# Kernel optimization log

Hardware: AMD Instinct MI355X
Metric: run time of the kernel (lower is better)

## Reference

```python
import jax, jax.numpy as jnp
import numpy as np

N = 100000   # nodes
E = 1600000  # edges
DIN, H, C = 64, 64, 40


def setup_inputs() -> dict:
    key = jax.random.key(0)
    ks = jax.random.split(key, 8)
    x = jax.random.normal(ks[0], (N, DIN), dtype=jnp.float32)
    edge_index = jax.random.randint(ks[1], (2, E), 0, N, dtype=jnp.int64)
    def glorot(k, fan_in, fan_out):
        s = jnp.sqrt(6.0 / (fan_in + fan_out)).astype(jnp.float32)
        return jax.random.uniform(k, (fan_in, fan_out), jnp.float32, -s, s)
    return {
        "x": x,
        "edge_index": edge_index,
        "W1": glorot(ks[2], DIN, H), "b1": jnp.zeros((H,), jnp.float32),
        "W2": glorot(ks[3], H, H),   "b2": jnp.zeros((H,), jnp.float32),
        "W3": glorot(ks[4], H, C),   "b3": jnp.zeros((C,), jnp.float32),
    }


def _gcn_norm(edge_index, n_nodes):
    # PyG GCNConv default: add self-loops, symmetric normalization.
    loop = jnp.arange(n_nodes, dtype=edge_index.dtype)
    src = jnp.concatenate([edge_index[0], loop])  # [E+N]
    dst = jnp.concatenate([edge_index[1], loop])
    deg = jax.ops.segment_sum(jnp.ones_like(dst, dtype=jnp.float32), dst,
                              num_segments=n_nodes)
    dinv = jnp.where(deg > 0, jax.lax.rsqrt(deg), 0.0)
    norm = dinv[src] * dinv[dst]  # [E+N]
    return src, dst, norm


def _gcn_conv(x, src, dst, norm, W, b, n_nodes):
    h = x @ W                                   # [N, F_out] tiny GEMM
    msg = h[src] * norm[:, None]                # gather + scale  [E+N, F_out]
    out = jax.ops.segment_sum(msg, dst, num_segments=n_nodes)  # scatter-add
    return out + b


def reference(x, edge_index, W1, b1, W2, b2, W3, b3):
    n = x.shape[0]
    src, dst, norm = _gcn_norm(edge_index, n)
    h = jax.nn.relu(_gcn_conv(x, src, dst, norm, W1, b1, n))
    # dropout(p=0.5) is identity in eval mode
    h = jax.nn.relu(_gcn_conv(h, src, dst, norm, W2, b2, n))
    return _gcn_conv(h, src, dst, norm, W3, b3, n)
```

## Files before the change

### kernel.cpp

```cpp
#include <hip/hip_runtime.h>
#include <hip/hip_fp16.h>

#define NN 100000
#define NE 1600000
#define NPAD 100352
#define ST 68
#define SXS 68
#define NB 256
#define CE (NE / NB)
#define D1 391
#define L1 (D1 * NB)


__global__ __launch_bounds__(256) void k_hist(const int* __restrict__ dst,
                                              unsigned* __restrict__ H) {
    __shared__ unsigned h[D1];
    int b = blockIdx.x, t = threadIdx.x;
    for (int i = t; i < D1; i += 256) h[i] = 0;
    __syncthreads();
    int beg = b * CE, end = beg + CE;
    for (int i = beg + t; i < end; i += 256)
        atomicAdd(&h[((unsigned)dst[i]) >> 8], 1u);
    __syncthreads();
    for (int d = t; d < D1; d += 256) H[d * NB + b] = h[d];
}

__global__ __launch_bounds__(256) void k_scanA(const unsigned* __restrict__ in,
                                               unsigned* __restrict__ bsum, int L) {
    __shared__ unsigned sp[256];
    int i = blockIdx.x * 256 + threadIdx.x;
    sp[threadIdx.x] = (i < L) ? in[i] : 0;
    __syncthreads();
    for (int off = 128; off > 0; off >>= 1) {
        if (threadIdx.x < off) sp[threadIdx.x] += sp[threadIdx.x + off];
        __syncthreads();
    }
    if (threadIdx.x == 0) bsum[blockIdx.x] = sp[0];
}

__global__ __launch_bounds__(512) void k_scanB(unsigned* __restrict__ bsum, int nb) {
    __shared__ unsigned sp[512];
    int t = threadIdx.x;
    unsigned v = (t < nb) ? bsum[t] : 0;
    sp[t] = v;
    __syncthreads();
    for (int off = 1; off < 512; off <<= 1) {
        unsigned u = (t >= off) ? sp[t - off] : 0;
        __syncthreads();
        sp[t] += u;
        __syncthreads();
    }
    if (t < nb) bsum[t] = sp[t] - v;
}

__global__ __launch_bounds__(256) void k_scanC(unsigned* __restrict__ H,
                                               const unsigned* __restrict__ bsum, int L) {
    __shared__ unsigned sp[256];
    int t = threadIdx.x, i = blockIdx.x * 256 + t;
    unsigned v = (i < L) ? H[i] : 0;
    sp[t] = v;
    __syncthreads();
    for (int off = 1; off < 256; off <<= 1) {
        unsigned u = (t >= off) ? sp[t - off] : 0;
        __syncthreads();
        sp[t] += u;
        __syncthreads();
    }
    if (i < L) H[i] = bsum[blockIdx.x] + sp[t] - v;
}

__global__ __launch_bounds__(256) void k_scat(const int* __restrict__ src,
                                              const int* __restrict__ dst,
                                              const unsigned* __restrict__ H,
                                              unsigned* __restrict__ pairs) {
    __shared__ unsigned base[D1];
    __shared__ unsigned run[D1];
    int b = blockIdx.x, t = threadIdx.x;
    for (int d = t; d < D1; d += 256) { base[d] = H[d * NB + b]; run[d] = 0; }
    __syncthreads();
    int beg = b * CE, end = beg + CE;
    for (int i = beg + t; i < end; i += 256) {
        unsigned dv = (unsigned)dst[i];
        unsigned d = dv >> 8;
        unsigned r = atomicAdd(&run[d], 1u);
        pairs[base[d] + r] = ((dv & 255u) << 24) | (unsigned)src[i];
    }
}

__global__ __launch_bounds__(256) void k_bucket(const unsigned* __restrict__ H,
                                                const unsigned* __restrict__ pairs,
                                                int* __restrict__ rowptr,
                                                float* __restrict__ dinv,
                                                int* __restrict__ csr) {
    __shared__ unsigned h[256], sc[256], run[256];
    int b = blockIdx.x, t = threadIdx.x;
    unsigned S = H[b * NB];
    unsigned Send = (b + 1 < D1) ? H[(b + 1) * NB] : NE;
    h[t] = 0; run[t] = 0;
    __syncthreads();
    for (unsigned i = S + t; i < Send; i += 256)
        atomicAdd(&h[pairs[i] >> 24], 1u);
    __syncthreads();
    unsigned v = h[t];
    sc[t] = v;
    __syncthreads();
    for (int off = 1; off < 256; off <<= 1) {
        unsigned u = (t >= off) ? sc[t - off] : 0;
        __syncthreads();
        sc[t] += u;
        __syncthreads();
    }
    unsigned ex = sc[t] - v;
    int node = (b << 8) + t;
    if (node < NN) {
        rowptr[node] = (int)(S + ex);
        dinv[node] = rsqrtf((float)v + 1.0f);
    }
    if (b == 0 && t == 0) rowptr[NN] = NE;
    sc[t] = ex;
    __syncthreads();
    for (unsigned i = S + t; i < Send; i += 256) {
        unsigned p = pairs[i];
        unsigned k = p >> 24;
        unsigned r = atomicAdd(&run[k], 1u);
        csr[S + sc[k] + r] = (int)(p & 0xFFFFFFu);
    }
}


__global__ __launch_bounds__(256, 4) void k_gemm1(const float* __restrict__ A,
                                                  const float* __restrict__ W,
                                                  const float* __restrict__ dinv,
                                                  __half* __restrict__ out, int n) {
    __shared__ float sX[32 * SXS];
    __shared__ float sW[64 * 64];
    int row0 = blockIdx.x * 32;
    for (int i = threadIdx.x; i < 16 * 64; i += 256)
        ((float4*)sW)[i] = ((const float4*)W)[i];
    for (int i = threadIdx.x; i < 32 * 16; i += 256) {
        int r = i >> 4, c4 = i & 15;
        int row = row0 + r;
        float4 v = (row < n) ? ((const float4*)(A + ((size_t)row << 6)))[c4]
                             : make_float4(0.f, 0.f, 0.f, 0.f);
        *(float4*)&sX[r * SXS + (c4 << 2)] = v;
    }
    __syncthreads();

    int ci = (threadIdx.x & 15) * 4;
    int r0 = (threadIdx.x >> 4) * 2;
    float acc[2][4] = {};
#pragma unroll 16
    for (int k = 0; k < 64; ++k) {
        float a0 = sX[r0 * SXS + k];
        float a1 = sX[(r0 + 1) * SXS + k];
        float4 w = *(const float4*)&sW[(k << 6) + ci];
        acc[0][0] += a0 * w.x; acc[0][1] += a0 * w.y;
        acc[0][2] += a0 * w.z; acc[0][3] += a0 * w.w;
        acc[1][0] += a1 * w.x; acc[1][1] += a1 * w.y;
        acc[1][2] += a1 * w.z; acc[1][3] += a1 * w.w;
    }
#pragma unroll
    for (int rr = 0; rr < 2; ++rr) {
        int row = row0 + r0 + rr;
        if (row < n) {
            float di = dinv[row];
            union { uint2 u; __half2 h[2]; } P;
            P.h[0] = __float22half2_rn(make_float2(acc[rr][0] * di, acc[rr][1] * di));
            P.h[1] = __float22half2_rn(make_float2(acc[rr][2] * di, acc[rr][3] * di));
            *(uint2*)(out + ((size_t)row << 6) + ci) = P.u;
        }
    }
}


#define ACC8(r) { \
    const __half2* hh_ = (const __half2*)&(r); \
    float2 f_; \
    f_ = __half22float2(hh_[0]); a[0].x += f_.x; a[0].y += f_.y; \
    f_ = __half22float2(hh_[1]); a[1].x += f_.x; a[1].y += f_.y; \
    f_ = __half22float2(hh_[2]); a[2].x += f_.x; a[2].y += f_.y; \
    f_ = __half22float2(hh_[3]); a[3].x += f_.x; a[3].y += f_.y; }

template <int MODE>
__global__ __launch_bounds__(256) void k_agg(const int* __restrict__ rowptr,
                                             const int* __restrict__ csr,
                                             const __half* __restrict__ g,
                                             const float* __restrict__ dinv,
                                             const float* __restrict__ bias,
                                             const float* __restrict__ Wn,
                                             const float* __restrict__ bias2,
                                             void* __restrict__ outv, int n) {
    constexpr int M = (MODE == 3) ? 40 : 64;
    __shared__ float sW[(MODE >= 2) ? 64 * M : 1];
    __shared__ float sT[(MODE >= 2) ? 32 * ST : 1];
    int tid = threadIdx.x;
    if (MODE >= 2) {
        for (int i = tid; i < 16 * M; i += 256)
            ((float4*)sW)[i] = ((const float4*)Wn)[i];
    }
    int n0 = blockIdx.x << 5;
    int lane = tid & 63, wid = tid >> 6;
    int ng = lane >> 3, fl = lane & 7;
    int nl = (wid << 3) + ng;
    int node = n0 + nl;
    bool valid = node < n;
    const uint4* g4 = (const uint4*)g;

    int beg = 0, end = 0;
    if (valid) { beg = rowptr[node]; end = rowptr[node + 1]; }
    float2 a[4] = {};
    int j = beg;
    for (; j + 4 <= end; j += 4) {
        int s0 = csr[j], s1 = csr[j + 1], s2 = csr[j + 2], s3 = csr[j + 3];
        uint4 r0 = g4[((size_t)s0 << 3) + fl];
        uint4 r1 = g4[((size_t)s1 << 3) + fl];
        uint4 r2 = g4[((size_t)s2 << 3) + fl];
        uint4 r3 = g4[((size_t)s3 << 3) + fl];
        ACC8(r0); ACC8(r1); ACC8(r2); ACC8(r3);
    }
    for (; j < end; ++j) {
        int s = csr[j];
        uint4 r = g4[((size_t)s << 3) + fl];
        ACC8(r);
    }
    if (valid) {
        uint4 r = g4[((size_t)node << 3) + fl];
        ACC8(r);
    }
    float di = valid ? dinv[node] : 0.f;
    float t[8] = { a[0].x, a[0].y, a[1].x, a[1].y, a[2].x, a[2].y, a[3].x, a[3].y };

    if (MODE == 1) {
        if (valid) {
            float4 b0 = *(const float4*)(bias + (fl << 3));
            float4 b1 = *(const float4*)(bias + (fl << 3) + 4);
            float bv[8] = { b0.x, b0.y, b0.z, b0.w, b1.x, b1.y, b1.z, b1.w };
            union { uint4 u; __half2 h[4]; } P;
#pragma unroll
            for (int k = 0; k < 4; ++k) {
                float o0 = fmaxf(t[2 * k]     * di + bv[2 * k],     0.f) * di;
                float o1 = fmaxf(t[2 * k + 1] * di + bv[2 * k + 1], 0.f) * di;
                P.h[k] = __float22half2_rn(make_float2(o0, o1));
            }
            ((uint4*)outv)[((size_t)node << 3) + fl] = P.u;
        }
        return;
    }

    {
        float4 b0 = make_float4(0.f, 0.f, 0.f, 0.f), b1 = b0;
        if (MODE == 2) {
            b0 = *(const float4*)(bias + (fl << 3));
            b1 = *(const float4*)(bias + (fl << 3) + 4);
        }
        float bv[8] = { b0.x, b0.y, b0.z, b0.w, b1.x, b1.y, b1.z, b1.w };
        float* row = &sT[nl * ST + (fl << 3)];
#pragma unroll
        for (int k = 0; k < 8; ++k) {
            float v = t[k] * di;
            if (MODE == 2) v = fmaxf(v + bv[k], 0.f);
            row[k] = v;
        }
    }
    __syncthreads();

    int rg = tid >> 4;
    int cq = (tid & 15) << 2;
    if (cq < M) {
        float s0[4] = {}, s1[4] = {};
#pragma unroll 8
        for (int k = 0; k < 64; ++k) {
            float4 w = *(const float4*)&sW[k * M + cq];
            float a0 = sT[(rg * 2) * ST + k];
            float a1 = sT[(rg * 2 + 1) * ST + k];
            s0[0] += a0 * w.x; s0[1] += a0 * w.y; s0[2] += a0 * w.z; s0[3] += a0 * w.w;
            s1[0] += a1 * w.x; s1[1] += a1 * w.y; s1[2] += a1 * w.z; s1[3] += a1 * w.w;
        }
#pragma unroll
        for (int r = 0; r < 2; ++r) {
            float* s = (r == 0) ? s0 : s1;
            int node2 = n0 + rg * 2 + r;
            if (node2 < n) {
                if (MODE == 2) {
                    float d2 = dinv[node2];
                    union { uint2 u; __half2 h[2]; } P;
                    P.h[0] = __float22half2_rn(make_float2(s[0] * d2, s[1] * d2));
                    P.h[1] = __float22half2_rn(make_float2(s[2] * d2, s[3] * d2));
                    *(uint2*)((__half*)outv + ((size_t)node2 << 6) + cq) = P.u;
                } else {
                    float4 o = make_float4(s[0] + bias2[cq],     s[1] + bias2[cq + 1],
                                           s[2] + bias2[cq + 2], s[3] + bias2[cq + 3]);
                    *(float4*)((float*)outv + (size_t)node2 * 40 + cq) = o;
                }
            }
        }
    }
}

extern "C" void kernel_launch(void* const* d_in, const int* in_sizes, int n_in,
                              void* d_out, int out_size, void* d_ws, size_t ws_size,
                              hipStream_t stream) {
    const float* x  = (const float*)d_in[0];
    const int*   ei = (const int*)d_in[1];
    const float* W1 = (const float*)d_in[2];
    const float* b1 = (const float*)d_in[3];
    const float* W2 = (const float*)d_in[4];
    const float* b2 = (const float*)d_in[5];
    const float* W3 = (const float*)d_in[6];
    const float* b3 = (const float*)d_in[7];
    float* out = (float*)d_out;

    const int* src = ei;
    const int* dst = ei + NE;

    unsigned* H      = (unsigned*)d_ws;
    unsigned* bsum   = H + L1;
    int*      rowptr = (int*)(bsum + 512);
    float*    dinv   = (float*)(rowptr + NPAD);
    unsigned* pairs  = (unsigned*)(dinv + NPAD);
    int*      csr    = (int*)(pairs + NE);
    __half*   gA     = (__half*)(csr + NE);
    __half*   gB     = gA + (size_t)NN * 64;

    const int B = 256;
    const int gG = (NN + 31) / 32;
    const int gAgg = (NN + 31) / 32;
    const int nScan = (L1 + 255) / 256;

    k_hist<<<NB, B, 0, stream>>>(dst, H);
    k_scanA<<<nScan, B, 0, stream>>>(H, bsum, L1);
    k_scanB<<<1, 512, 0, stream>>>(bsum, nScan);
    k_scanC<<<nScan, B, 0, stream>>>(H, bsum, L1);
    k_scat<<<NB, B, 0, stream>>>(src, dst, H, pairs);
    k_bucket<<<D1, B, 0, stream>>>(H, pairs, rowptr, dinv, csr);

    k_gemm1<<<gG, B, 0, stream>>>(x, W1, dinv, gA, NN);
    k_agg<2><<<gAgg, B, 0, stream>>>(rowptr, csr, gA, dinv, b1, W2, nullptr, gB, NN);
    k_agg<1><<<gAgg, B, 0, stream>>>(rowptr, csr, gB, dinv, b2, nullptr, nullptr, gA, NN);
    k_agg<3><<<gAgg, B, 0, stream>>>(rowptr, csr, gA, dinv, nullptr, W3, b3, out, NN);
}
```

Baseline: 184.5 us.

## Degree-sort nodes within buckets to balance aggregation work and unroll gathers by eight

k_bucket now bitonic-sorts the 256 nodes of each bucket by in-degree and emits a permutation plus per-position begin/end edge ranges. The three aggregation kernels walk nodes in that order, so nodes of similar degree share a wavefront and lanes diverge less, and the output rows are scattered through the permutation. The gather loop is also unrolled to 8 edges to keep more loads in flight. The costs are a sort inside the bucket kernel, an extra indirection, and scattered writes that no longer land on contiguous rows.

```diff
diff --git a/kernel.cpp b/kernel.cpp
--- a/kernel.cpp
+++ b/kernel.cpp
@@ -91,8 +91,10 @@
                                                 const unsigned* __restrict__ pairs,
                                                 int* __restrict__ rowptr,
                                                 float* __restrict__ dinv,
-                                                int* __restrict__ csr) {
-    __shared__ unsigned h[256], sc[256], run[256];
+                                                int* __restrict__ csr,
+                                                int* __restrict__ order,
+                                                int2* __restrict__ begend) {
+    __shared__ unsigned h[256], sc[256], run[256], key[256];
     int b = blockIdx.x, t = threadIdx.x;
     unsigned S = H[b * NB];
     unsigned Send = (b + 1 < D1) ? H[(b + 1) * NB] : NE;
@@ -118,6 +120,7 @@
     }
     if (b == 0 && t == 0) rowptr[NN] = NE;
     sc[t] = ex;
+    key[t] = (node < NN) ? ((v << 8) | (unsigned)t) : 0xFFFFFFFFu;
     __syncthreads();
     for (unsigned i = S + t; i < Send; i += 256) {
         unsigned p = pairs[i];
@@ -125,6 +128,25 @@
         unsigned r = atomicAdd(&run[k], 1u);
         csr[S + sc[k] + r] = (int)(p & 0xFFFFFFu);
     }
+    for (int kk = 2; kk <= 256; kk <<= 1) {
+        for (int jj = kk >> 1; jj > 0; jj >>= 1) {
+            __syncthreads();
+            int p = t ^ jj;
+            if (p > t) {
+                unsigned a = key[t], c = key[p];
+                bool up = ((t & kk) == 0);
+                if ((a > c) == up) { key[t] = c; key[p] = a; }
+            }
+        }
+    }
+    __syncthreads();
+    unsigned kv = key[t];
+    int nl2 = (int)(kv & 255u);
+    int dg = (int)(kv >> 8);
+    int pos = (b << 8) + t;
+    order[pos] = (b << 8) + nl2;
+    int bg = (int)(S + sc[nl2]);
+    begend[pos] = make_int2(bg, bg + dg);
 }
 
 
@@ -182,7 +204,8 @@
     f_ = __half22float2(hh_[3]); a[3].x += f_.x; a[3].y += f_.y; }
 
 template <int MODE>
-__global__ __launch_bounds__(256) void k_agg(const int* __restrict__ rowptr,
+__global__ __launch_bounds__(256) void k_agg(const int* __restrict__ order,
+                                             const int2* __restrict__ begend,
                                              const int* __restrict__ csr,
                                              const __half* __restrict__ g,
                                              const float* __restrict__ dinv,
@@ -202,21 +225,40 @@
     int lane = tid & 63, wid = tid >> 6;
     int ng = lane >> 3, fl = lane & 7;
     int nl = (wid << 3) + ng;
-    int node = n0 + nl;
-    bool valid = node < n;
+    int pos = n0 + nl;
+    bool valid = pos < n;
+    int node = 0, beg = 0, end = 0;
+    if (valid) {
+        node = order[pos];
+        int2 be = begend[pos];
+        beg = be.x; end = be.y;
+    }
     const uint4* g4 = (const uint4*)g;
 
-    int beg = 0, end = 0;
-    if (valid) { beg = rowptr[node]; end = rowptr[node + 1]; }
     float2 a[4] = {};
     int j = beg;
-    for (; j + 4 <= end; j += 4) {
+    for (; j + 8 <= end; j += 8) {
+        int s0 = csr[j],     s1 = csr[j + 1], s2 = csr[j + 2], s3 = csr[j + 3];
+        int s4 = csr[j + 4], s5 = csr[j + 5], s6 = csr[j + 6], s7 = csr[j + 7];
+        uint4 r0 = g4[((size_t)s0 << 3) + fl];
+        uint4 r1 = g4[((size_t)s1 << 3) + fl];
+        uint4 r2 = g4[((size_t)s2 << 3) + fl];
+        uint4 r3 = g4[((size_t)s3 << 3) + fl];
+        uint4 r4 = g4[((size_t)s4 << 3) + fl];
+        uint4 r5 = g4[((size_t)s5 << 3) + fl];
+        uint4 r6 = g4[((size_t)s6 << 3) + fl];
+        uint4 r7 = g4[((size_t)s7 << 3) + fl];
+        ACC8(r0); ACC8(r1); ACC8(r2); ACC8(r3);
+        ACC8(r4); ACC8(r5); ACC8(r6); ACC8(r7);
+    }
+    if (j + 4 <= end) {
         int s0 = csr[j], s1 = csr[j + 1], s2 = csr[j + 2], s3 = csr[j + 3];
         uint4 r0 = g4[((size_t)s0 << 3) + fl];
         uint4 r1 = g4[((size_t)s1 << 3) + fl];
         uint4 r2 = g4[((size_t)s2 << 3) + fl];
         uint4 r3 = g4[((size_t)s3 << 3) + fl];
         ACC8(r0); ACC8(r1); ACC8(r2); ACC8(r3);
+        j += 4;
     }
     for (; j < end; ++j) {
         int s = csr[j];
@@ -279,8 +321,9 @@
 #pragma unroll
         for (int r = 0; r < 2; ++r) {
             float* s = (r == 0) ? s0 : s1;
-            int node2 = n0 + rg * 2 + r;
-            if (node2 < n) {
+            int pos2 = n0 + rg * 2 + r;
+            if (pos2 < n) {
+                int node2 = order[pos2];
                 if (MODE == 2) {
                     float d2 = dinv[node2];
                     union { uint2 u; __half2 h[2]; } P;
@@ -317,7 +360,9 @@
     unsigned* bsum   = H + L1;
     int*      rowptr = (int*)(bsum + 512);
     float*    dinv   = (float*)(rowptr + NPAD);
-    unsigned* pairs  = (unsigned*)(dinv + NPAD);
+    int*      order  = (int*)(dinv + NPAD);
+    int2*     begend = (int2*)(order + NPAD);
+    unsigned* pairs  = (unsigned*)(begend + NPAD);
     int*      csr    = (int*)(pairs + NE);
     __half*   gA     = (__half*)(csr + NE);
     __half*   gB     = gA + (size_t)NN * 64;
@@ -332,10 +377,10 @@
     k_scanB<<<1, 512, 0, stream>>>(bsum, nScan);
     k_scanC<<<nScan, B, 0, stream>>>(H, bsum, L1);
     k_scat<<<NB, B, 0, stream>>>(src, dst, H, pairs);
-    k_bucket<<<D1, B, 0, stream>>>(H, pairs, rowptr, dinv, csr);
+    k_bucket<<<D1, B, 0, stream>>>(H, pairs, rowptr, dinv, csr, order, begend);
 
     k_gemm1<<<gG, B, 0, stream>>>(x, W1, dinv, gA, NN);
-    k_agg<2><<<gAgg, B, 0, stream>>>(rowptr, csr, gA, dinv, b1, W2, nullptr, gB, NN);
-    k_agg<1><<<gAgg, B, 0, stream>>>(rowptr, csr, gB, dinv, b2, nullptr, nullptr, gA, NN);
-    k_agg<3><<<gAgg, B, 0, stream>>>(rowptr, csr, gA, dinv, nullptr, W3, b3, out, NN);
-}
+    k_agg<2><<<gAgg, B, 0, stream>>>(order, begend, csr, gA, dinv, b1, W2, nullptr, gB, NN);
+    k_agg<1><<<gAgg, B, 0, stream>>>(order, begend, csr, gB, dinv, b2, nullptr, nullptr, gA, NN);
+    k_agg<3><<<gAgg, B, 0, stream>>>(order, begend, csr, gA, dinv, nullptr, W3, b3, out, NN);
+}
```

New measurement: 206.7 us. 12.1% more time.

## Apply W3 before final aggregation to gather 40-wide rows instead of 64

Applied to the files above, without the earlier changes.

Reorders the last layer so the W3 projection is fused into the second aggregation kernel, producing a 40-wide half-precision intermediate. A new aggregation kernel then gathers the narrower 40-feature rows and adds the bias, cutting the gather traffic of the last layer. The cost is that 3 of 8 lanes per node sit idle in the final gather, and rows are 80 bytes, which are not 128-byte aligned. It also needs an extra workspace buffer.

```diff
diff --git a/kernel.cpp b/kernel.cpp
--- a/kernel.cpp
+++ b/kernel.cpp
@@ -181,23 +181,19 @@
     f_ = __half22float2(hh_[2]); a[2].x += f_.x; a[2].y += f_.y; \
     f_ = __half22float2(hh_[3]); a[3].x += f_.x; a[3].y += f_.y; }
 
-template <int MODE>
-__global__ __launch_bounds__(256) void k_agg(const int* __restrict__ rowptr,
-                                             const int* __restrict__ csr,
-                                             const __half* __restrict__ g,
-                                             const float* __restrict__ dinv,
-                                             const float* __restrict__ bias,
-                                             const float* __restrict__ Wn,
-                                             const float* __restrict__ bias2,
-                                             void* __restrict__ outv, int n) {
-    constexpr int M = (MODE == 3) ? 40 : 64;
-    __shared__ float sW[(MODE >= 2) ? 64 * M : 1];
-    __shared__ float sT[(MODE >= 2) ? 32 * ST : 1];
+template <int M>
+__global__ __launch_bounds__(256) void k_agg64(const int* __restrict__ rowptr,
+                                               const int* __restrict__ csr,
+                                               const __half* __restrict__ g,
+                                               const float* __restrict__ dinv,
+                                               const float* __restrict__ bias,
+                                               const float* __restrict__ Wn,
+                                               __half* __restrict__ outh, int n) {
+    __shared__ float sW[64 * M];
+    __shared__ float sT[32 * ST];
     int tid = threadIdx.x;
-    if (MODE >= 2) {
-        for (int i = tid; i < 16 * M; i += 256)
-            ((float4*)sW)[i] = ((const float4*)Wn)[i];
-    }
+    for (int i = tid; i < 16 * M; i += 256)
+        ((float4*)sW)[i] = ((const float4*)Wn)[i];
     int n0 = blockIdx.x << 5;
     int lane = tid & 63, wid = tid >> 6;
     int ng = lane >> 3, fl = lane & 7;
@@ -230,37 +226,14 @@
     float di = valid ? dinv[node] : 0.f;
     float t[8] = { a[0].x, a[0].y, a[1].x, a[1].y, a[2].x, a[2].y, a[3].x, a[3].y };
 
-    if (MODE == 1) {
-        if (valid) {
-            float4 b0 = *(const float4*)(bias + (fl << 3));
-            float4 b1 = *(const float4*)(bias + (fl << 3) + 4);
-            float bv[8] = { b0.x, b0.y, b0.z, b0.w, b1.x, b1.y, b1.z, b1.w };
-            union { uint4 u; __half2 h[4]; } P;
-#pragma unroll
-            for (int k = 0; k < 4; ++k) {
-                float o0 = fmaxf(t[2 * k]     * di + bv[2 * k],     0.f) * di;
-                float o1 = fmaxf(t[2 * k + 1] * di + bv[2 * k + 1], 0.f) * di;
-                P.h[k] = __float22half2_rn(make_float2(o0, o1));
-            }
-            ((uint4*)outv)[((size_t)node << 3) + fl] = P.u;
-        }
-        return;
-    }
-
     {
-        float4 b0 = make_float4(0.f, 0.f, 0.f, 0.f), b1 = b0;
-        if (MODE == 2) {
-            b0 = *(const float4*)(bias + (fl << 3));
-            b1 = *(const float4*)(bias + (fl << 3) + 4);
-        }
+        float4 b0 = *(const float4*)(bias + (fl << 3));
+        float4 b1 = *(const float4*)(bias + (fl << 3) + 4);
         float bv[8] = { b0.x, b0.y, b0.z, b0.w, b1.x, b1.y, b1.z, b1.w };
         float* row = &sT[nl * ST + (fl << 3)];
 #pragma unroll
-        for (int k = 0; k < 8; ++k) {
-            float v = t[k] * di;
-            if (MODE == 2) v = fmaxf(v + bv[k], 0.f);
-            row[k] = v;
-        }
+        for (int k = 0; k < 8; ++k)
+            row[k] = fmaxf(t[k] * di + bv[k], 0.f);
     }
     __syncthreads();
 
@@ -281,19 +254,62 @@
             float* s = (r == 0) ? s0 : s1;
             int node2 = n0 + rg * 2 + r;
             if (node2 < n) {
-                if (MODE == 2) {
-                    float d2 = dinv[node2];
-                    union { uint2 u; __half2 h[2]; } P;
-                    P.h[0] = __float22half2_rn(make_float2(s[0] * d2, s[1] * d2));
-                    P.h[1] = __float22half2_rn(make_float2(s[2] * d2, s[3] * d2));
-                    *(uint2*)((__half*)outv + ((size_t)node2 << 6) + cq) = P.u;
-                } else {
-                    float4 o = make_float4(s[0] + bias2[cq],     s[1] + bias2[cq + 1],
-                                           s[2] + bias2[cq + 2], s[3] + bias2[cq + 3]);
-                    *(float4*)((float*)outv + (size_t)node2 * 40 + cq) = o;
-                }
+                float d2 = dinv[node2];
+                union { uint2 u; __half2 h[2]; } P;
+                P.h[0] = __float22half2_rn(make_float2(s[0] * d2, s[1] * d2));
+                P.h[1] = __float22half2_rn(make_float2(s[2] * d2, s[3] * d2));
+                *(uint2*)(outh + (size_t)node2 * M + cq) = P.u;
             }
         }
+    }
+}
+
+
+__global__ __launch_bounds__(256) void k_agg40(const int* __restrict__ rowptr,
+                                               const int* __restrict__ csr,
+                                               const __half* __restrict__ q,
+                                               const float* __restrict__ dinv,
+                                               const float* __restrict__ bias,
+                                               float* __restrict__ out, int n) {
+    int tid = threadIdx.x;
+    int n0 = blockIdx.x << 5;
+    int lane = tid & 63, wid = tid >> 6;
+    int ng = lane >> 3, fl = lane & 7;
+    int nl = (wid << 3) + ng;
+    int node = n0 + nl;
+    bool valid = (node < n) && (fl < 5);
+
+    int beg = 0, end = 0;
+    if (valid) { beg = rowptr[node]; end = rowptr[node + 1]; }
+    float2 a[4] = {};
+    int j = beg;
+    for (; j + 4 <= end; j += 4) {
+        int s0 = csr[j], s1 = csr[j + 1], s2 = csr[j + 2], s3 = csr[j + 3];
+        uint4 r0 = *(const uint4*)(q + (size_t)s0 * 40 + (fl << 3));
+        uint4 r1 = *(const uint4*)(q + (size_t)s1 * 40 + (fl << 3));
+        uint4 r2 = *(const uint4*)(q + (size_t)s2 * 40 + (fl << 3));
+        uint4 r3 = *(const uint4*)(q + (size_t)s3 * 40 + (fl << 3));
+        ACC8(r0); ACC8(r1); ACC8(r2); ACC8(r3);
+    }
+    for (; j < end; ++j) {
+        int s = csr[j];
+        uint4 r = *(const uint4*)(q + (size_t)s * 40 + (fl << 3));
+        ACC8(r);
+    }
+    if (valid) {
+        uint4 r = *(const uint4*)(q + (size_t)node * 40 + (fl << 3));
+        ACC8(r);
+        float di = dinv[node];
+        float t[8] = { a[0].x, a[0].y, a[1].x, a[1].y, a[2].x, a[2].y, a[3].x, a[3].y };
+        float4 b0 = *(const float4*)(bias + (fl << 3));
+        float4 b1 = *(const float4*)(bias + (fl << 3) + 4);
+        float4 o0 = make_float4(t[0] * di + b0.x, t[1] * di + b0.y,
+                                t[2] * di + b0.z, t[3] * di + b0.w);
+        float4 o1 = make_float4(t[4] * di + b1.x, t[5] * di + b1.y,
+                                t[6] * di + b1.z, t[7] * di + b1.w);
+        float* op = out + (size_t)node * 40 + (fl << 3);
+        *(float4*)op = o0;
+        *(float4*)(op + 4) = o1;
     }
 }
 
@@ -321,6 +337,7 @@
     int*      csr    = (int*)(pairs + NE);
     __half*   gA     = (__half*)(csr + NE);
     __half*   gB     = gA + (size_t)NN * 64;
+    __half*   gC     = gB + (size_t)NN * 64;
 
     const int B = 256;
     const int gG = (NN + 31) / 32;
@@ -335,7 +352,7 @@
     k_bucket<<<D1, B, 0, stream>>>(H, pairs, rowptr, dinv, csr);
 
     k_gemm1<<<gG, B, 0, stream>>>(x, W1, dinv, gA, NN);
-    k_agg<2><<<gAgg, B, 0, stream>>>(rowptr, csr, gA, dinv, b1, W2, nullptr, gB, NN);
-    k_agg<1><<<gAgg, B, 0, stream>>>(rowptr, csr, gB, dinv, b2, nullptr, nullptr, gA, NN);
-    k_agg<3><<<gAgg, B, 0, stream>>>(rowptr, csr, gA, dinv, nullptr, W3, b3, out, NN);
-}
+    k_agg64<64><<<gAgg, B, 0, stream>>>(rowptr, csr, gA, dinv, b1, W2, gB, NN);
+    k_agg64<40><<<gAgg, B, 0, stream>>>(rowptr, csr, gB, dinv, b2, W3, gC, NN);
+    k_agg40<<<gAgg, B, 0, stream>>>(rowptr, csr, gC, dinv, b3, out, NN);
+}
```

New measurement: 184.8 us (median of 2 runs). About the same (+0.2%).
